# Performance work log

Hardware: AMD Instinct MI355X
Metric: run time of the kernel (lower is better)

Reference implementation:

```python
import jax, jax.numpy as jnp
import numpy as np

N = 50000      # nodes
E = 400000     # edges per hop
IN = 256       # in_channels
H = 4          # heads
C = 64         # out_channels per head
NEG = 0.2      # leaky relu negative slope


def setup_inputs() -> dict:
    key = jax.random.key(0)
    ks = jax.random.split(key, 10)
    x = jax.random.normal(ks[0], (N, IN), dtype=jnp.float32)
    edge_index1 = jax.random.randint(ks[1], (2, E), 0, N, dtype=jnp.int32)
    edge_index2 = jax.random.randint(ks[2], (2, E), 0, N, dtype=jnp.int32)
    s = 0.05
    Wl0 = jax.random.normal(ks[3], (IN, H * C), dtype=jnp.float32) * s
    Wr0 = jax.random.normal(ks[4], (IN, H * C), dtype=jnp.float32) * s
    att0 = jax.random.normal(ks[5], (H, C), dtype=jnp.float32) * s
    Wl1 = jax.random.normal(ks[6], (IN, H * C), dtype=jnp.float32) * s
    Wr1 = jax.random.normal(ks[7], (IN, H * C), dtype=jnp.float32) * s
    att1 = jax.random.normal(ks[8], (H, C), dtype=jnp.float32) * s
    return {"x": x, "Wl0": Wl0, "Wr0": Wr0, "att0": att0,
            "Wl1": Wl1, "Wr1": Wr1, "att1": att1,
            "edge_index1": edge_index1, "edge_index2": edge_index2}


def _gatv2_hop(x, Wl, Wr, att, src, dst):
    """One GATv2Conv hop (bias=False, residual=False, eval-mode dropout, concat=False)."""
    n = x.shape[0]
    xl = (x @ Wl).reshape(n, H, C)   # source-side projection
    xr = (x @ Wr).reshape(n, H, C)   # target-side projection
    # edge-wise GATv2 score: a^T leaky_relu(x_l[j] + x_r[i])
    m = jax.nn.leaky_relu(xl[src] + xr[dst], NEG)            # [E, H, C]
    e = jnp.einsum('ehc,hc->eh', m, att)                     # [E, H]
    # segment softmax over incoming edges of each destination node
    e_max = jax.lax.stop_gradient(
        jax.ops.segment_max(e, dst, num_segments=n))         # [N, H]
    ex = jnp.exp(e - e_max[dst])
    denom = jax.ops.segment_sum(ex, dst, num_segments=n)     # [N, H]
    alpha = ex / (denom[dst] + 1e-16)                        # [E, H]
    msg = xl[src] * alpha[:, :, None]                        # [E, H, C]
    out = jax.ops.segment_sum(msg, dst, num_segments=n)      # [N, H, C]
    return out.mean(axis=1)                                  # concat=False -> mean heads


def reference(x, Wl0, Wr0, att0, Wl1, Wr1, att1, edge_index1, edge_index2):
    n = x.shape[0]
    # hop 0: add_self_loops=True
    loop = jnp.arange(n, dtype=edge_index1.dtype)
    src0 = jnp.concatenate([edge_index1[0], loop])
    dst0 = jnp.concatenate([edge_index1[1], loop])
    out = _gatv2_hop(x, Wl0, Wr0, att0, src0, dst0)
    # hop 1: no self loops, scaled by 1/(k+1) = 1/2
    out = out + _gatv2_hop(x, Wl1, Wr1, att1, edge_index2[0], edge_index2[1]) / 2.0
    return out
```

## Files before the change

kernel.cpp:

```cpp
#include <hip/hip_runtime.h>

typedef unsigned int uint;
typedef unsigned short ushort;

typedef __bf16 bf16x8 __attribute__((ext_vector_type(8)));
typedef float f32x4 __attribute__((ext_vector_type(4)));

#define CAP 48

__device__ __forceinline__ float bf2f(ushort u) {
    return __uint_as_float(((uint)u) << 16);
}
__device__ __forceinline__ ushort f2bf(float f) {
    uint u = __float_as_uint(f);
    u += 0x7fffu + ((u >> 16) & 1u);
    return (ushort)(u >> 16);
}
__device__ __forceinline__ float4 up4(ushort4 v) {
    return make_float4(bf2f(v.x), bf2f(v.y), bf2f(v.z), bf2f(v.w));
}
__device__ __forceinline__ float lrelu(float v) {
    return v > 0.f ? v : 0.2f * v;
}
__device__ __forceinline__ void load_lds16(const ushort* g, ushort* l) {
    __builtin_amdgcn_global_load_lds(
        (const __attribute__((address_space(1))) void*)g,
        (__attribute__((address_space(3))) void*)l, 16, 0, 0);
}
__device__ __forceinline__ int swz(int row) { return (row + (row >> 2)) & 3; }

__global__ __launch_bounds__(256) void convert_x(
    const float* __restrict__ X, ushort* __restrict__ Xb, int Nrows, int total8)
{
    int i = blockIdx.x * 256 + threadIdx.x;
    if (i >= total8) return;
    int base = i * 8;
    int row = base >> 8;
    ushort o[8];
    if (row < Nrows) {
        float4 v0 = *(const float4*)(X + base);
        float4 v1 = *(const float4*)(X + base + 4);
        o[0] = f2bf(v0.x); o[1] = f2bf(v0.y); o[2] = f2bf(v0.z); o[3] = f2bf(v0.w);
        o[4] = f2bf(v1.x); o[5] = f2bf(v1.y); o[6] = f2bf(v1.z); o[7] = f2bf(v1.w);
    } else {
#pragma unroll
        for (int j = 0; j < 8; j++) o[j] = 0;
    }
    *(uint4*)(Xb + base) = *(const uint4*)o;
}

__global__ __launch_bounds__(256) void convert_w(
    const float* __restrict__ Wl0, const float* __restrict__ Wr0,
    const float* __restrict__ Wl1, const float* __restrict__ Wr1,
    ushort* __restrict__ Wt)
{
    int n = blockIdx.x;
    int k = threadIdx.x;
    const float* W = (n < 256) ? Wl0 : (n < 512) ? Wr0 : (n < 768) ? Wl1 : Wr1;
    Wt[n * 256 + k] = f2bf(W[k * 256 + (n & 255)]);
}

__global__ __launch_bounds__(256, 2) void gemm_mfma(
    const ushort* __restrict__ Xb,
    const ushort* __restrict__ Wt,
    ushort* __restrict__ XL,
    ushort* __restrict__ XR,
    int Nrows)
{
    __shared__ ushort As[128 * 32];
    __shared__ ushort Bs[128 * 32];

    const int tid = threadIdx.x;
    const int w = tid >> 6, l = tid & 63;
    const int wm = w & 1, wn = w >> 1;
    const int m0 = blockIdx.y * 128;
    const int n0g = blockIdx.x * 128;

    f32x4 acc[4][4];
#pragma unroll
    for (int i = 0; i < 4; i++)
#pragma unroll
        for (int j = 0; j < 4; j++) acc[i][j] = (f32x4)(0.f);

    const int fr = l & 15, fq = l >> 4;
    int a_off[4], b_off[4];
#pragma unroll
    for (int t = 0; t < 4; t++) {
        int rA = wm * 64 + t * 16 + fr;
        a_off[t] = (rA * 4 + ((fq + swz(rA)) & 3)) * 8;
        int rB = wn * 64 + t * 16 + fr;
        b_off[t] = (rB * 4 + ((fq + swz(rB)) & 3)) * 8;
    }

    for (int k0 = 0; k0 < 256; k0 += 32) {
        __syncthreads();
#pragma unroll
        for (int r = 0; r < 2; r++) {
            int slot = r * 256 + tid;
            int row = slot >> 2;
            int kp = ((slot & 3) - swz(row)) & 3;
            load_lds16(Xb + (size_t)(m0 + row) * 256 + k0 + kp * 8,
                       &As[(r * 256 + w * 64) * 8]);
            load_lds16(Wt + (size_t)(n0g + row) * 256 + k0 + kp * 8,
                       &Bs[(r * 256 + w * 64) * 8]);
        }
        __syncthreads();

        bf16x8 a[4], b[4];
#pragma unroll
        for (int t = 0; t < 4; t++) {
            a[t] = *(const bf16x8*)(As + a_off[t]);
            b[t] = *(const bf16x8*)(Bs + b_off[t]);
        }
#pragma unroll
        for (int mi = 0; mi < 4; mi++)
#pragma unroll
            for (int ni = 0; ni < 4; ni++)
                acc[mi][ni] = __builtin_amdgcn_mfma_f32_16x16x32_bf16(
                    a[mi], b[ni], acc[mi][ni], 0, 0, 0);
    }

    const bool left = (n0g < 256);
    ushort* OUT = left ? XL : XR;
    const int cbase = (n0g & 255) + wn * 64 + fr;
#pragma unroll
    for (int mi = 0; mi < 4; mi++) {
#pragma unroll
        for (int reg = 0; reg < 4; reg++) {
            int row = m0 + wm * 64 + mi * 16 + fq * 4 + reg;
            if (row >= Nrows) continue;
#pragma unroll
            for (int ni = 0; ni < 4; ni++) {
                OUT[(size_t)row * 256 + cbase + ni * 16] = f2bf(acc[mi][ni][reg]);
            }
        }
    }
}

__global__ __launch_bounds__(256) void csr_init(
    int* __restrict__ cnt, int* __restrict__ srcs, int N, int self)
{
    int d = blockIdx.x * 256 + threadIdx.x;
    if (d >= N) return;
    cnt[d] = self ? 1 : 0;
    if (self) srcs[(size_t)d * CAP] = d;
}

__global__ __launch_bounds__(256) void csr_scatter(
    const int* __restrict__ src, const int* __restrict__ dst,
    int* __restrict__ cnt, int* __restrict__ srcs, int E)
{
    int e = blockIdx.x * 256 + threadIdx.x;
    if (e >= E) return;
    int d = dst[e];
    int pos = atomicAdd(&cnt[d], 1);
    if (pos < CAP) srcs[(size_t)d * CAP + pos] = src[e];
}

__device__ __forceinline__ ushort4 gat_load(const ushort* __restrict__ XLb,
                                            int s, int lane) {
    return *(const ushort4*)(XLb + (size_t)s * 256 + lane * 4);
}
__device__ __forceinline__ void edge_accum(ushort4 raw, float4 xr, float4 av,
        float& a0, float& a1, float& a2, float& a3, float& den) {
    float4 xa = up4(raw);
    float p = av.x * lrelu(xa.x + xr.x) + av.y * lrelu(xa.y + xr.y)
            + av.z * lrelu(xa.z + xr.z) + av.w * lrelu(xa.w + xr.w);
    p += __shfl_xor(p, 1);
    p += __shfl_xor(p, 2);
    p += __shfl_xor(p, 4);
    p += __shfl_xor(p, 8);
    float exv = __expf(p);
    den += exv;
    a0 = fmaf(exv, xa.x, a0);
    a1 = fmaf(exv, xa.y, a1);
    a2 = fmaf(exv, xa.z, a2);
    a3 = fmaf(exv, xa.w, a3);
}

__global__ __launch_bounds__(256) void gat_aggregate(
    const ushort* __restrict__ XLb,
    const ushort* __restrict__ XRb,
    const float* __restrict__ att,
    const int* __restrict__ cnt,
    const int* __restrict__ srcs,
    const float* __restrict__ base,
    float* __restrict__ outp,
    float scale, int N)
{
    int d = blockIdx.x * 4 + (threadIdx.x >> 6);
    if (d >= N) return;
    int lane = threadIdx.x & 63;

    float4 xr = up4(*(const ushort4*)(XRb + (size_t)d * 256 + lane * 4));
    float4 av = *(const float4*)(att + lane * 4);

    int m = cnt[d];
    if (m > CAP) m = CAP;
    int sv = (lane < m) ? srcs[(size_t)d * CAP + lane] : 0;

    float a0 = 0.f, a1 = 0.f, a2 = 0.f, a3 = 0.f, den = 0.f;

    if (m > 0) {
        const int c = m - 1;
        ushort4 p0, p1, p2, p3;
        p0 = gat_load(XLb, __shfl(sv, 0), lane);
        if (1 <= c) p1 = gat_load(XLb, __shfl(sv, 1), lane);
        if (2 <= c) p2 = gat_load(XLb, __shfl(sv, 2), lane);
        if (3 <= c) p3 = gat_load(XLb, __shfl(sv, 3), lane);
        for (int i = 0; i < m; i += 4) {
            ushort4 c0 = p0, c1 = p1, c2 = p2, c3 = p3;
            int b = i + 4;
            if (b     <= c) p0 = gat_load(XLb, __shfl(sv, b),     lane);
            if (b + 1 <= c) p1 = gat_load(XLb, __shfl(sv, b + 1), lane);
            if (b + 2 <= c) p2 = gat_load(XLb, __shfl(sv, b + 2), lane);
            if (b + 3 <= c) p3 = gat_load(XLb, __shfl(sv, b + 3), lane);
            edge_accum(c0, xr, av, a0, a1, a2, a3, den);
            if (i + 1 < m) edge_accum(c1, xr, av, a0, a1, a2, a3, den);
            if (i + 2 < m) edge_accum(c2, xr, av, a0, a1, a2, a3, den);
            if (i + 3 < m) edge_accum(c3, xr, av, a0, a1, a2, a3, den);
        }
    }

    float inv = scale / (den + 1e-16f);
    float v0 = a0 * inv, v1 = a1 * inv, v2 = a2 * inv, v3 = a3 * inv;
    v0 += __shfl_xor(v0, 16); v0 += __shfl_xor(v0, 32);
    v1 += __shfl_xor(v1, 16); v1 += __shfl_xor(v1, 32);
    v2 += __shfl_xor(v2, 16); v2 += __shfl_xor(v2, 32);
    v3 += __shfl_xor(v3, 16); v3 += __shfl_xor(v3, 32);
    int jsel = lane >> 4;
    float vv = (jsel == 0) ? v0 : (jsel == 1) ? v1 : (jsel == 2) ? v2 : v3;
    int ch = ((lane & 15) << 2) + jsel;
    float prev = base ? base[(size_t)d * 64 + ch] : 0.f;
    outp[(size_t)d * 64 + ch] = prev + vv;
}

extern "C" void kernel_launch(void* const* d_in, const int* in_sizes, int n_in,
                              void* d_out, int out_size, void* d_ws, size_t ws_size,
                              hipStream_t stream)
{
    const float* x    = (const float*)d_in[0];
    const float* Wl0  = (const float*)d_in[1];
    const float* Wr0  = (const float*)d_in[2];
    const float* att0 = (const float*)d_in[3];
    const float* Wl1  = (const float*)d_in[4];
    const float* Wr1  = (const float*)d_in[5];
    const float* att1 = (const float*)d_in[6];
    const int* ei1 = (const int*)d_in[7];
    const int* ei2 = (const int*)d_in[8];

    const int N  = in_sizes[0] / 256;
    const int E1 = in_sizes[7] / 2;
    const int E2 = in_sizes[8] / 2;
    const int Mpad = ((N + 127) / 128) * 128;

    char* ws = (char*)d_ws;
    size_t off = 0;
    ushort* Xb  = (ushort*)(ws + off); off += (size_t)Mpad * 256 * sizeof(ushort);
    ushort* Wt  = (ushort*)(ws + off); off += (size_t)1024 * 256 * sizeof(ushort);
    ushort* XL  = (ushort*)(ws + off); off += (size_t)N * 256 * sizeof(ushort);
    ushort* XR  = (ushort*)(ws + off); off += (size_t)N * 256 * sizeof(ushort);
    int* cnt    = (int*)(ws + off);    off += (size_t)N * sizeof(int);
    int* srcs   = (int*)(ws + off);    off += (size_t)N * CAP * sizeof(int);
    float* outf = (float*)d_out;
    ushort* Wt0 = Wt;
    ushort* Wt1 = Wt + (size_t)512 * 256;

    int nblkN = (N + 255) / 256;

    int total8 = Mpad * 256 / 8;
    convert_x<<<(total8 + 255) / 256, 256, 0, stream>>>(x, Xb, N, total8);
    convert_w<<<1024, 256, 0, stream>>>(Wl0, Wr0, Wl1, Wr1, Wt);

    dim3 ggrid(4, Mpad / 128);
    int aggblk = (N + 3) / 4;

    gemm_mfma<<<ggrid, 256, 0, stream>>>(Xb, Wt0, XL, XR, N);
    csr_init<<<nblkN, 256, 0, stream>>>(cnt, srcs, N, 1);
    csr_scatter<<<(E1 + 255) / 256, 256, 0, stream>>>(ei1, ei1 + E1, cnt, srcs, E1);
    gat_aggregate<<<aggblk, 256, 0, stream>>>(XL, XR, att0, cnt, srcs,
                                              nullptr, outf, 0.25f, N);
    gemm_mfma<<<ggrid, 256, 0, stream>>>(Xb, Wt1, XL, XR, N);
    csr_init<<<nblkN, 256, 0, stream>>>(cnt, srcs, N, 0);
    csr_scatter<<<(E2 + 255) / 256, 256, 0, stream>>>(ei2, ei2 + E2, cnt, srcs, E2);
    gat_aggregate<<<aggblk, 256, 0, stream>>>(XL, XR, att1, cnt, srcs,
                                              outf, outf, 0.125f, N);
}
```

Baseline: 313.7 us.

## Merge prep kernels, batch both CSR builds, fuse both-hop GEMMs, deepen gather prefetch

Merges the x/weight conversion and CSR initialization into one prep kernel, and builds both hops' CSR lists in a single scatter launch using separate count and source buffers. When the workspace is large enough, one GEMM launch with twice the column blocks produces all four projections at once, followed by the two aggregations. The aggregation prefetch depth grows from 4 to 8 rows. This removes launch gaps and small serialized kernels and gives the GEMM a bigger grid, at the cost of more workspace and higher register use in the aggregation kernel.

```diff
diff --git a/kernel.cpp b/kernel.cpp
--- a/kernel.cpp
+++ b/kernel.cpp
@@ -29,42 +29,72 @@
 }
 __device__ __forceinline__ int swz(int row) { return (row + (row >> 2)) & 3; }
 
-__global__ __launch_bounds__(256) void convert_x(
-    const float* __restrict__ X, ushort* __restrict__ Xb, int Nrows, int total8)
-{
-    int i = blockIdx.x * 256 + threadIdx.x;
-    if (i >= total8) return;
-    int base = i * 8;
-    int row = base >> 8;
-    ushort o[8];
-    if (row < Nrows) {
-        float4 v0 = *(const float4*)(X + base);
-        float4 v1 = *(const float4*)(X + base + 4);
-        o[0] = f2bf(v0.x); o[1] = f2bf(v0.y); o[2] = f2bf(v0.z); o[3] = f2bf(v0.w);
-        o[4] = f2bf(v1.x); o[5] = f2bf(v1.y); o[6] = f2bf(v1.z); o[7] = f2bf(v1.w);
-    } else {
-#pragma unroll
-        for (int j = 0; j < 8; j++) o[j] = 0;
-    }
-    *(uint4*)(Xb + base) = *(const uint4*)o;
-}
-
-__global__ __launch_bounds__(256) void convert_w(
+__global__ __launch_bounds__(256) void prep(
+    const float* __restrict__ X, ushort* __restrict__ Xb, int Nrows, int Mpad,
     const float* __restrict__ Wl0, const float* __restrict__ Wr0,
     const float* __restrict__ Wl1, const float* __restrict__ Wr1,
-    ushort* __restrict__ Wt)
-{
-    int n = blockIdx.x;
-    int k = threadIdx.x;
-    const float* W = (n < 256) ? Wl0 : (n < 512) ? Wr0 : (n < 768) ? Wl1 : Wr1;
-    Wt[n * 256 + k] = f2bf(W[k * 256 + (n & 255)]);
+    ushort* __restrict__ Wt,
+    int* __restrict__ cnt0, int* __restrict__ srcs0, int* __restrict__ cnt1)
+{
+    const int BX = Mpad / 8;
+    int blk = blockIdx.x;
+    if (blk < BX) {
+        int i = blk * 256 + threadIdx.x;
+        int base = i * 8;
+        int row = base >> 8;
+        ushort o[8];
+        if (row < Nrows) {
+            float4 v0 = *(const float4*)(X + base);
+            float4 v1 = *(const float4*)(X + base + 4);
+            o[0] = f2bf(v0.x); o[1] = f2bf(v0.y); o[2] = f2bf(v0.z); o[3] = f2bf(v0.w);
+            o[4] = f2bf(v1.x); o[5] = f2bf(v1.y); o[6] = f2bf(v1.z); o[7] = f2bf(v1.w);
+        } else {
+#pragma unroll
+            for (int j = 0; j < 8; j++) o[j] = 0;
+        }
+        *(uint4*)(Xb + base) = *(const uint4*)o;
+        return;
+    }
+    blk -= BX;
+    if (blk < 1024) {
+        int n = blk;
+        int k = threadIdx.x;
+        const float* W = (n < 256) ? Wl0 : (n < 512) ? Wr0 : (n < 768) ? Wl1 : Wr1;
+        Wt[n * 256 + k] = f2bf(W[k * 256 + (n & 255)]);
+        return;
+    }
+    blk -= 1024;
+    int d = blk * 256 + threadIdx.x;
+    if (d < Nrows) {
+        cnt0[d] = 1;
+        srcs0[(size_t)d * CAP] = d;
+        cnt1[d] = 0;
+    }
+}
+
+__global__ __launch_bounds__(256) void csr_scatter2(
+    const int* __restrict__ ei1, const int* __restrict__ ei2,
+    int* __restrict__ cnt0, int* __restrict__ srcs0,
+    int* __restrict__ cnt1, int* __restrict__ srcs1,
+    int E1, int E2)
+{
+    int e = blockIdx.x * 256 + threadIdx.x;
+    if (e < E1) {
+        int d = ei1[E1 + e];
+        int pos = atomicAdd(&cnt0[d], 1);
+        if (pos < CAP) srcs0[(size_t)d * CAP + pos] = ei1[e];
+    } else if (e < E1 + E2) {
+        int e2 = e - E1;
+        int d = ei2[E2 + e2];
+        int pos = atomicAdd(&cnt1[d], 1);
+        if (pos < CAP) srcs1[(size_t)d * CAP + pos] = ei2[e2];
+    }
 }
 
 __global__ __launch_bounds__(256, 2) void gemm_mfma(
     const ushort* __restrict__ Xb,
     const ushort* __restrict__ Wt,
-    ushort* __restrict__ XL,
-    ushort* __restrict__ XR,
+    ushort* __restrict__ XP,
     int Nrows)
 {
     __shared__ ushort As[128 * 32];
@@ -120,8 +150,7 @@
                     a[mi], b[ni], acc[mi][ni], 0, 0, 0);
     }
 
-    const bool left = (n0g < 256);
-    ushort* OUT = left ? XL : XR;
+    ushort* OUT = XP + (size_t)(n0g >> 8) * ((size_t)Nrows * 256);
     const int cbase = (n0g & 255) + wn * 64 + fr;
 #pragma unroll
     for (int mi = 0; mi < 4; mi++) {
@@ -135,26 +164,6 @@
             }
         }
     }
-}
-
-__global__ __launch_bounds__(256) void csr_init(
-    int* __restrict__ cnt, int* __restrict__ srcs, int N, int self)
-{
-    int d = blockIdx.x * 256 + threadIdx.x;
-    if (d >= N) return;
-    cnt[d] = self ? 1 : 0;
-    if (self) srcs[(size_t)d * CAP] = d;
-}
-
-__global__ __launch_bounds__(256) void csr_scatter(
-    const int* __restrict__ src, const int* __restrict__ dst,
-    int* __restrict__ cnt, int* __restrict__ srcs, int E)
-{
-    int e = blockIdx.x * 256 + threadIdx.x;
-    if (e >= E) return;
-    int d = dst[e];
-    int pos = atomicAdd(&cnt[d], 1);
-    if (pos < CAP) srcs[(size_t)d * CAP + pos] = src[e];
 }
 
 __device__ __forceinline__ ushort4 gat_load(const ushort* __restrict__ XLb,
@@ -203,22 +212,21 @@
 
     if (m > 0) {
         const int c = m - 1;
-        ushort4 p0, p1, p2, p3;
-        p0 = gat_load(XLb, __shfl(sv, 0), lane);
-        if (1 <= c) p1 = gat_load(XLb, __shfl(sv, 1), lane);
-        if (2 <= c) p2 = gat_load(XLb, __shfl(sv, 2), lane);
-        if (3 <= c) p3 = gat_load(XLb, __shfl(sv, 3), lane);
-        for (int i = 0; i < m; i += 4) {
-            ushort4 c0 = p0, c1 = p1, c2 = p2, c3 = p3;
-            int b = i + 4;
-            if (b     <= c) p0 = gat_load(XLb, __shfl(sv, b),     lane);
-            if (b + 1 <= c) p1 = gat_load(XLb, __shfl(sv, b + 1), lane);
-            if (b + 2 <= c) p2 = gat_load(XLb, __shfl(sv, b + 2), lane);
-            if (b + 3 <= c) p3 = gat_load(XLb, __shfl(sv, b + 3), lane);
-            edge_accum(c0, xr, av, a0, a1, a2, a3, den);
-            if (i + 1 < m) edge_accum(c1, xr, av, a0, a1, a2, a3, den);
-            if (i + 2 < m) edge_accum(c2, xr, av, a0, a1, a2, a3, den);
-            if (i + 3 < m) edge_accum(c3, xr, av, a0, a1, a2, a3, den);
+        ushort4 p[8];
+#pragma unroll
+        for (int j = 0; j < 8; j++)
+            if (j <= c) p[j] = gat_load(XLb, __shfl(sv, j), lane);
+        for (int i = 0; i < m; i += 8) {
+            ushort4 cur[8];
+#pragma unroll
+            for (int j = 0; j < 8; j++) cur[j] = p[j];
+            int b = i + 8;
+#pragma unroll
+            for (int j = 0; j < 8; j++)
+                if (b + j <= c) p[j] = gat_load(XLb, __shfl(sv, b + j), lane);
+#pragma unroll
+            for (int j = 0; j < 8; j++)
+                if (i + j < m) edge_accum(cur[j], xr, av, a0, a1, a2, a3, den);
         }
     }
 
@@ -253,36 +261,41 @@
     const int E1 = in_sizes[7] / 2;
     const int E2 = in_sizes[8] / 2;
     const int Mpad = ((N + 127) / 128) * 128;
+    const size_t NB = (size_t)N * 256;
 
     char* ws = (char*)d_ws;
     size_t off = 0;
     ushort* Xb  = (ushort*)(ws + off); off += (size_t)Mpad * 256 * sizeof(ushort);
     ushort* Wt  = (ushort*)(ws + off); off += (size_t)1024 * 256 * sizeof(ushort);
-    ushort* XL  = (ushort*)(ws + off); off += (size_t)N * 256 * sizeof(ushort);
-    ushort* XR  = (ushort*)(ws + off); off += (size_t)N * 256 * sizeof(ushort);
-    int* cnt    = (int*)(ws + off);    off += (size_t)N * sizeof(int);
-    int* srcs   = (int*)(ws + off);    off += (size_t)N * CAP * sizeof(int);
+    int* cnt0   = (int*)(ws + off);    off += (size_t)N * sizeof(int);
+    int* cnt1   = (int*)(ws + off);    off += (size_t)N * sizeof(int);
+    int* srcs0  = (int*)(ws + off);    off += (size_t)N * CAP * sizeof(int);
+    int* srcs1  = (int*)(ws + off);    off += (size_t)N * CAP * sizeof(int);
+    ushort* XP  = (ushort*)(ws + off);
+    size_t need_mega = off + 4 * NB * sizeof(ushort);
+    const bool mega = (ws_size >= need_mega);
     float* outf = (float*)d_out;
-    ushort* Wt0 = Wt;
-    ushort* Wt1 = Wt + (size_t)512 * 256;
-
-    int nblkN = (N + 255) / 256;
-
-    int total8 = Mpad * 256 / 8;
-    convert_x<<<(total8 + 255) / 256, 256, 0, stream>>>(x, Xb, N, total8);
-    convert_w<<<1024, 256, 0, stream>>>(Wl0, Wr0, Wl1, Wr1, Wt);
-
-    dim3 ggrid(4, Mpad / 128);
+
+    const int BX = Mpad / 8;
+    int prep_blocks = BX + 1024 + (N + 255) / 256;
+    prep<<<prep_blocks, 256, 0, stream>>>(x, Xb, N, Mpad, Wl0, Wr0, Wl1, Wr1,
+                                          Wt, cnt0, srcs0, cnt1);
+    csr_scatter2<<<(E1 + E2 + 255) / 256, 256, 0, stream>>>(
+        ei1, ei2, cnt0, srcs0, cnt1, srcs1, E1, E2);
+
     int aggblk = (N + 3) / 4;
-
-    gemm_mfma<<<ggrid, 256, 0, stream>>>(Xb, Wt0, XL, XR, N);
-    csr_init<<<nblkN, 256, 0, stream>>>(cnt, srcs, N, 1);
-    csr_scatter<<<(E1 + 255) / 256, 256, 0, stream>>>(ei1, ei1 + E1, cnt, srcs, E1);
-    gat_aggregate<<<aggblk, 256, 0, stream>>>(XL, XR, att0, cnt, srcs,
-                                              nullptr, outf, 0.25f, N);
-    gemm_mfma<<<ggrid, 256, 0, stream>>>(Xb, Wt1, XL, XR, N);
-    csr_init<<<nblkN, 256, 0, stream>>>(cnt, srcs, N, 0);
-    csr_scatter<<<(E2 + 255) / 256, 256, 0, stream>>>(ei2, ei2 + E2, cnt, srcs, E2);
-    gat_aggregate<<<aggblk, 256, 0, stream>>>(XL, XR, att1, cnt, srcs,
-                                              outf, outf, 0.125f, N);
-}
+    if (mega) {
+        gemm_mfma<<<dim3(8, Mpad / 128), 256, 0, stream>>>(Xb, Wt, XP, N);
+        gat_aggregate<<<aggblk, 256, 0, stream>>>(XP, XP + NB, att0, cnt0, srcs0,
+                                                  nullptr, outf, 0.25f, N);
+        gat_aggregate<<<aggblk, 256, 0, stream>>>(XP + 2 * NB, XP + 3 * NB, att1,
+                                                  cnt1, srcs1, outf, outf, 0.125f, N);
+    } else {
+        gemm_mfma<<<dim3(4, Mpad / 128), 256, 0, stream>>>(Xb, Wt, XP, N);
+        gat_aggregate<<<aggblk, 256, 0, stream>>>(XP, XP + NB, att0, cnt0, srcs0,
+                                                  nullptr, outf, 0.25f, N);
+        gemm_mfma<<<dim3(4, Mpad / 128), 256, 0, stream>>>(Xb, Wt + 512 * 256, XP, N);
+        gat_aggregate<<<aggblk, 256, 0, stream>>>(XP, XP + NB, att1, cnt1, srcs1,
+                                                  outf, outf, 0.125f, N);
+    }
+}
```

Result: faster. 297.9 us (-5.0%).
